# Kernel optimization log

Hardware: AMD Instinct MI355X
Metric: run time of the kernel (lower is better)

Reference implementation:

```python
import jax, jax.numpy as jnp
import numpy as np

N_NEURONS = 100000
NNZ = 3200000
N_SENSORY = 5000
BATCH = 16
NUM_LAYERS = 8
THRESHOLD = 0.01
TANH_STEEPNESS = 5.0


def setup_inputs() -> dict:
    key = jax.random.key(0)
    k1, k2, k3, k4 = jax.random.split(key, 4)
    inputs = jax.random.uniform(k1, (BATCH, N_SENSORY, NUM_LAYERS), dtype=jnp.float32)
    # sparse connectome in COO form; small values so activations stay in a sane range
    weight_vals = jax.random.normal(k2, (NNZ,), dtype=jnp.float32) * 0.1
    weight_rows = jax.random.randint(k3, (NNZ,), 0, N_NEURONS, dtype=jnp.int32)
    weight_cols = jax.random.randint(k4, (NNZ,), 0, N_NEURONS, dtype=jnp.int32)
    sensory_indices = jnp.arange(N_SENSORY, dtype=jnp.int32)
    return {
        "inputs": inputs,
        "weight_vals": weight_vals,
        "weight_rows": weight_rows,
        "weight_cols": weight_cols,
        "sensory_indices": sensory_indices,
    }


def _spmm(vals, rows, cols, x):
    # x: (N, B); y[r, b] = sum_{e: rows[e]==r} vals[e] * x[cols[e], b]
    return jax.ops.segment_sum(vals[:, None] * x[cols], rows, num_segments=N_NEURONS)


def _activate(y):
    y = jnp.where(y >= THRESHOLD, y, jnp.zeros_like(y))
    return jnp.tanh(TANH_STEEPNESS * y)


def reference(inputs, weight_vals, weight_rows, weight_cols, sensory_indices):
    B, S, T = inputs.shape  # T == num_layers
    # preprocess sensory input: threshold then clamp to <= 1
    inp = jnp.where(inputs >= THRESHOLD, inputs, jnp.zeros_like(inputs))
    inp = jnp.minimum(inp, jnp.ones_like(inp))
    # state x: (N, B)
    full_input = jnp.zeros((N_NEURONS, B), inputs.dtype).at[sensory_indices].add(inp[:, :, 0].T)
    x = _activate(_spmm(weight_vals, weight_rows, weight_cols, full_input))
    acts = []
    for layer in range(1, T):
        # inject sensory input for this time step and clamp to <= 1
        x = x.at[sensory_indices].add(inp[:, :, layer].T)
        x = jnp.minimum(x, jnp.ones_like(x))
        acts.append(x)
        x = _activate(_spmm(weight_vals, weight_rows, weight_cols, x))
    acts.append(x)  # last layer: no injection
    # (T, N, B) -> (B, N, T), matching torch vmap'd cat along time dim
    return jnp.stack(acts, axis=0).transpose(2, 1, 0)
```

## Files before the change

### kernel.cpp

```cpp
#include <hip/hip_runtime.h>


#define N_NEURONS 100000
#define NNZ_CNT   3200000
#define N_SENSORY 5000
#define BATCH     16
#define T_LAYERS  8
#define THRESH    0.01f
#define STEEP     5.0f

#define NB (N_NEURONS * BATCH)
#define NT (N_NEURONS * T_LAYERS)
#define ST (N_SENSORY * T_LAYERS)

#define FXS32     134217728.0f
#define FXI32     7.450580596923828e-9f

#define LBITS   9
#define BROWS   (1 << LBITS)
#define NBUCKET ((N_NEURONS + BROWS - 1) / BROWS)
#define EPB     4096
#define NBLK_A  ((NNZ_CNT + EPB - 1) / EPB)

#define FXSCALE   17592186044416.0f
#define FXINV     (1.0 / 17592186044416.0)

__device__ __forceinline__ float thresh_clamp_inp(float u) {
    u = (u >= THRESH) ? u : 0.0f;
    return fminf(u, 1.0f);
}
__device__ __forceinline__ float activate(float y) {
    y = (y >= THRESH) ? y : 0.0f;
    return tanhf(STEEP * y);
}


__global__ void k_init(const float* __restrict__ inp, float* __restrict__ state0,
                       int* __restrict__ btotal) {
    int i = blockIdx.x * blockDim.x + threadIdx.x;
    if (i >= NB) return;
    int n = i >> 4, b = i & 15;
    float v = 0.0f;
    if (n < N_SENSORY) v = thresh_clamp_inp(inp[b * ST + n * T_LAYERS + 0]);
    state0[i] = v;
    if (i < NBUCKET) btotal[i] = 0;
}

__global__ void __launch_bounds__(1024) k_bcount(const int* __restrict__ rows,
                                                 int* __restrict__ btotal) {
    __shared__ int cnt[NBUCKET];
    const int e0 = blockIdx.x * EPB;
    for (int i = threadIdx.x; i < NBUCKET; i += 1024) cnt[i] = 0;
    __syncthreads();
    #pragma unroll
    for (int i = 0; i < EPB / 1024; ++i) {
        int e = e0 + i * 1024 + threadIdx.x;
        if (e < NNZ_CNT) atomicAdd(&cnt[rows[e] >> LBITS], 1);
    }
    __syncthreads();
    for (int i = threadIdx.x; i < NBUCKET; i += 1024)
        if (cnt[i]) atomicAdd(&btotal[i], cnt[i]);
}

__global__ void k_bscan(const int* __restrict__ btotal, int* __restrict__ bbase,
                        int* __restrict__ bcur, int* __restrict__ row_ptr) {
    __shared__ int lds[256];
    int tid = threadIdx.x;
    int v = (tid < NBUCKET) ? btotal[tid] : 0;
    lds[tid] = v;
    __syncthreads();
    for (int off = 1; off < 256; off <<= 1) {
        int add = (tid >= off) ? lds[tid - off] : 0;
        __syncthreads();
        lds[tid] += add;
        __syncthreads();
    }
    if (tid < NBUCKET) {
        bbase[tid] = lds[tid] - v;
        bcur[tid]  = lds[tid] - v;
    }
    if (tid == 0) { bbase[NBUCKET] = NNZ_CNT; row_ptr[N_NEURONS] = NNZ_CNT; }
}

__global__ void __launch_bounds__(1024) k_passA(const float* __restrict__ vals,
                                                const int* __restrict__ rows,
                                                const int* __restrict__ cols,
                                                int* bcur,
                                                int2* __restrict__ slab) {
    __shared__ int cnt[NBUCKET];
    __shared__ int base[NBUCKET];
    const int e0 = blockIdx.x * EPB;
    for (int i = threadIdx.x; i < NBUCKET; i += 1024) cnt[i] = 0;
    __syncthreads();
    #pragma unroll
    for (int i = 0; i < EPB / 1024; ++i) {
        int e = e0 + i * 1024 + threadIdx.x;
        if (e < NNZ_CNT) atomicAdd(&cnt[rows[e] >> LBITS], 1);
    }
    __syncthreads();
    for (int i = threadIdx.x; i < NBUCKET; i += 1024) {
        int c = cnt[i];
        base[i] = (c > 0) ? atomicAdd(&bcur[i], c) : 0;
        cnt[i] = 0;
    }
    __syncthreads();
    #pragma unroll
    for (int i = 0; i < EPB / 1024; ++i) {
        int e = e0 + i * 1024 + threadIdx.x;
        if (e < NNZ_CNT) {
            int r = rows[e];
            int k = r >> LBITS;
            int pos = base[k] + atomicAdd(&cnt[k], 1);
            slab[pos] = make_int2((cols[e] << LBITS) | (r & (BROWS - 1)),
                                  __float_as_int(vals[e] * FXS32));
        }
    }
}

__global__ void __launch_bounds__(1024) k_passB(const int* __restrict__ bbase,
                                                const int2* __restrict__ slab,
                                                int2* __restrict__ packed,
                                                int* __restrict__ row_ptr) {
    __shared__ int cnt[BROWS];
    __shared__ int scn[BROWS];
    const int tid = threadIdx.x;
    const int k  = blockIdx.x;
    const int r0 = k * BROWS;
    const int nr = min(BROWS, N_NEURONS - r0);
    const int P0 = bbase[k], P1 = bbase[k + 1];
    for (int i = tid; i < BROWS; i += 1024) cnt[i] = 0;
    __syncthreads();
    for (int i = P0 + tid; i < P1; i += 1024)
        atomicAdd(&cnt[slab[i].x & (BROWS - 1)], 1);
    __syncthreads();
    if (tid < BROWS) scn[tid] = cnt[tid];
    __syncthreads();
    for (int off = 1; off < BROWS; off <<= 1) {
        int add = (tid < BROWS && tid >= off) ? scn[tid - off] : 0;
        __syncthreads();
        if (tid < BROWS) scn[tid] += add;
        __syncthreads();
    }
    if (tid < BROWS) {
        int ex = P0 + scn[tid] - cnt[tid];
        if (tid < nr) row_ptr[r0 + tid] = ex;
        scn[tid] = ex;
    }
    __syncthreads();
    for (int i = P0 + tid; i < P1; i += 1024) {
        int2 pe = slab[i];
        int d = atomicAdd(&scn[pe.x & (BROWS - 1)], 1);
        packed[d] = make_int2(pe.x >> LBITS, pe.y);
    }
}

__global__ void __launch_bounds__(256) k_layer(const int* __restrict__ row_ptr,
                                               const int2* __restrict__ packed,
                                               const float* __restrict__ state_in,
                                               const float* __restrict__ inp,
                                               float* __restrict__ plane_out,
                                               int t) {
    __shared__ int2 ebuf[16][17];
    const int tid = threadIdx.x;
    const int g = tid >> 4, b = tid & 15;
    const int r = blockIdx.x * 16 + g;
    const int s = row_ptr[r], e = row_ptr[r + 1];
    int acc = 0;
    for (int base = s; base < e; base += 16) {
        int idx = base + b;
        int2 pe = (idx < e) ? packed[idx] : make_int2(0, 0);
        ebuf[g][b] = pe;
        #pragma unroll
        for (int j = 0; j < 16; ++j) {
            int2 q = ebuf[g][j];
            float prod = __int_as_float(q.y) * state_in[q.x * BATCH + b];
            acc += __float2int_rn(prod);
        }
    }
    float y = (float)acc * FXI32;
    float a = activate(y);
    if (t < T_LAYERS - 1) {
        if (r < N_SENSORY) a += thresh_clamp_inp(inp[b * ST + r * T_LAYERS + (t + 1)]);
        a = fminf(a, 1.0f);
    }
    plane_out[r * BATCH + b] = a;
}

__global__ void k_out(const float* __restrict__ planes, float* __restrict__ out) {
    int i = blockIdx.x * blockDim.x + threadIdx.x;
    if (i >= NB) return;
    int n = i >> 4, b = i & 15;
    float4 o0, o1;
    o0.x = planes[0 * NB + i]; o0.y = planes[1 * NB + i];
    o0.z = planes[2 * NB + i]; o0.w = planes[3 * NB + i];
    o1.x = planes[4 * NB + i]; o1.y = planes[5 * NB + i];
    o1.z = planes[6 * NB + i]; o1.w = planes[7 * NB + i];
    float4* dst = (float4*)&out[b * NT + n * T_LAYERS];
    dst[0] = o0; dst[1] = o1;
}

__global__ void k2_init(const float* __restrict__ inp, float* __restrict__ state,
                        long long* __restrict__ acc) {
    int stride = gridDim.x * blockDim.x;
    for (int i = blockIdx.x * blockDim.x + threadIdx.x; i < NB; i += stride) {
        int n = i >> 4, b = i & 15;
        float v = 0.0f;
        if (n < N_SENSORY) v = thresh_clamp_inp(inp[b * ST + n * T_LAYERS + 0]);
        state[i] = v;
        acc[i]   = 0LL;
    }
}
__global__ void __launch_bounds__(256) k2_spmm(const float* __restrict__ vals,
                                               const int* __restrict__ rows,
                                               const int* __restrict__ cols,
                                               const float* __restrict__ state,
                                               long long* acc) {
    int tid = blockIdx.x * blockDim.x + threadIdx.x;
    int b = tid & 15;
    int e = tid >> 4;
    int estride = (gridDim.x * blockDim.x) >> 4;
    for (; e < NNZ_CNT; e += estride) {
        float xv = state[cols[e] * BATCH + b];
        long long fx = llrintf(vals[e] * xv * FXSCALE);
        if (fx != 0LL)
            atomicAdd((unsigned long long*)&acc[rows[e] * BATCH + b], (unsigned long long)fx);
    }
}
__global__ void k2_act_inject(long long* acc, const float* __restrict__ inp,
                              float* __restrict__ state, float* __restrict__ out, int t) {
    int stride = gridDim.x * blockDim.x;
    for (int i = blockIdx.x * blockDim.x + threadIdx.x; i < NB; i += stride) {
        int n = i >> 4, b = i & 15;
        float y = (float)((double)acc[i] * FXINV);
        acc[i] = 0LL;
        float v = activate(y);
        if (n < N_SENSORY) v += thresh_clamp_inp(inp[b * ST + n * T_LAYERS + (t + 1)]);
        v = fminf(v, 1.0f);
        state[i] = v;
        out[b * NT + n * T_LAYERS + t] = v;
    }
}
__global__ void k2_act_final(const long long* __restrict__ acc, float* __restrict__ out) {
    int stride = gridDim.x * blockDim.x;
    for (int i = blockIdx.x * blockDim.x + threadIdx.x; i < NB; i += stride) {
        int n = i >> 4, b = i & 15;
        float y = (float)((double)acc[i] * FXINV);
        out[b * NT + n * T_LAYERS + (T_LAYERS - 1)] = activate(y);
    }
}

extern "C" void kernel_launch(void* const* d_in, const int* in_sizes, int n_in,
                              void* d_out, int out_size, void* d_ws, size_t ws_size,
                              hipStream_t stream) {
    const float* inputs = (const float*)d_in[0];
    const float* vals   = (const float*)d_in[1];
    const int*   rows   = (const int*)  d_in[2];
    const int*   cols   = (const int*)  d_in[3];
    float* out = (float*)d_out;

    const size_t sz_planes = (size_t)T_LAYERS * NB * 4;
    const size_t sz_packed = (size_t)NNZ_CNT * 8;
    const size_t sz_rowptr = ((size_t)N_NEURONS + 2) * 4;
    const size_t sz_bt     = (size_t)(NBUCKET + 8) * 4;
    const size_t REQ = sz_planes + sz_packed + sz_rowptr + 3 * sz_bt;

    const int block = 256;

    if (ws_size >= REQ) {
        char* ws = (char*)d_ws;
        float* planes  = (float*)ws;
        int2*  packed  = (int2*)(ws + sz_planes);
        int*   row_ptr = (int*)(ws + sz_planes + sz_packed);
        int*   btotal  = (int*)(ws + sz_planes + sz_packed + sz_rowptr);
        int*   bbase   = (int*)(ws + sz_planes + sz_packed + sz_rowptr + sz_bt);
        int*   bcur    = (int*)(ws + sz_planes + sz_packed + sz_rowptr + 2 * sz_bt);
        float* state0  = planes + (size_t)(T_LAYERS - 1) * NB;
        int2*  slab    = (int2*)planes;

        const int grid_nb = (NB + block - 1) / block;

        k_init<<<grid_nb, block, 0, stream>>>(inputs, state0, btotal);
        k_bcount<<<NBLK_A, 1024, 0, stream>>>(rows, btotal);
        k_bscan<<<1, 256, 0, stream>>>(btotal, bbase, bcur, row_ptr);
        k_passA<<<NBLK_A, 1024, 0, stream>>>(vals, rows, cols, bcur, slab);
        k_passB<<<NBUCKET, 1024, 0, stream>>>(bbase, slab, packed, row_ptr);

        for (int t = 0; t < T_LAYERS; ++t) {
            const float* sin_ = (t == 0) ? state0 : planes + (size_t)(t - 1) * NB;
            k_layer<<<grid_nb, block, 0, stream>>>(row_ptr, packed, sin_, inputs,
                                                   planes + (size_t)t * NB, t);
        }
        k_out<<<grid_nb, block, 0, stream>>>(planes, out);
    } else {
        long long* acc   = (long long*)d_ws;
        float*     state = (float*)(acc + NB);
        const int grid_ew = 2048, grid_sp = 2048;
        k2_init<<<grid_ew, block, 0, stream>>>(inputs, state, acc);
        for (int t = 0; t < T_LAYERS; ++t) {
            k2_spmm<<<grid_sp, block, 0, stream>>>(vals, rows, cols, state, acc);
            if (t < T_LAYERS - 1)
                k2_act_inject<<<grid_ew, block, 0, stream>>>(acc, inputs, state, out, t);
            else
                k2_act_final<<<grid_ew, block, 0, stream>>>(acc, out);
        }
    }
}
```

Baseline: 400.8 us.

## Assign one wavefront per row in SpMM layer kernel with shuffle reduction

The layer kernel now maps a full 64-lane wavefront to each row. Four edge groups of 16 batch lanes each load edges directly from global memory, and their integer partial sums are combined with xor shuffles, replacing the shared-memory staging of 16 edges per 16-lane group. This is meant to give more memory-level parallelism per row (about 32 nonzeros per row) and remove the LDS round trips and padded iterations. In exchange it launches four times as many wavefronts per row, and only a quarter of the lanes do the final store.

```diff
diff --git a/kernel.cpp b/kernel.cpp
--- a/kernel.cpp
+++ b/kernel.cpp
@@ -160,30 +160,38 @@
                                                const float* __restrict__ inp,
                                                float* __restrict__ plane_out,
                                                int t) {
-    __shared__ int2 ebuf[16][17];
     const int tid = threadIdx.x;
-    const int g = tid >> 4, b = tid & 15;
-    const int r = blockIdx.x * 16 + g;
+    const int ln  = tid & 63;
+    const int jj  = ln >> 4;
+    const int b   = ln & 15;
+    const int r   = blockIdx.x * 4 + (tid >> 6);
     const int s = row_ptr[r], e = row_ptr[r + 1];
     int acc = 0;
-    for (int base = s; base < e; base += 16) {
-        int idx = base + b;
-        int2 pe = (idx < e) ? packed[idx] : make_int2(0, 0);
-        ebuf[g][b] = pe;
+    int base = s;
+    for (; base + 16 <= e; base += 16) {
         #pragma unroll
-        for (int j = 0; j < 16; ++j) {
-            int2 q = ebuf[g][j];
-            float prod = __int_as_float(q.y) * state_in[q.x * BATCH + b];
-            acc += __float2int_rn(prod);
-        }
-    }
-    float y = (float)acc * FXI32;
-    float a = activate(y);
-    if (t < T_LAYERS - 1) {
-        if (r < N_SENSORY) a += thresh_clamp_inp(inp[b * ST + r * T_LAYERS + (t + 1)]);
-        a = fminf(a, 1.0f);
-    }
-    plane_out[r * BATCH + b] = a;
+        for (int k = 0; k < 4; ++k) {
+            int2 q = packed[base + k * 4 + jj];
+            acc += __float2int_rn(__int_as_float(q.y) * state_in[(q.x << 4) + b]);
+        }
+    }
+    for (; base < e; base += 4) {
+        int idx = base + jj;
+        if (idx < e) {
+            int2 q = packed[idx];
+            acc += __float2int_rn(__int_as_float(q.y) * state_in[(q.x << 4) + b]);
+        }
+    }
+    acc += __shfl_xor(acc, 16, 64);
+    acc += __shfl_xor(acc, 32, 64);
+    if (jj == 0) {
+        float a = activate((float)acc * FXI32);
+        if (t < T_LAYERS - 1) {
+            if (r < N_SENSORY) a += thresh_clamp_inp(inp[b * ST + r * T_LAYERS + (t + 1)]);
+            a = fminf(a, 1.0f);
+        }
+        plane_out[(r << 4) + b] = a;
+    }
 }
 
 __global__ void k_out(const float* __restrict__ planes, float* __restrict__ out) {
@@ -278,6 +286,7 @@
         int2*  slab    = (int2*)planes;
 
         const int grid_nb = (NB + block - 1) / block;
+        const int grid_ly = N_NEURONS / 4;
 
         k_init<<<grid_nb, block, 0, stream>>>(inputs, state0, btotal);
         k_bcount<<<NBLK_A, 1024, 0, stream>>>(rows, btotal);
@@ -287,7 +296,7 @@
 
         for (int t = 0; t < T_LAYERS; ++t) {
             const float* sin_ = (t == 0) ? state0 : planes + (size_t)(t - 1) * NB;
-            k_layer<<<grid_nb, block, 0, stream>>>(row_ptr, packed, sin_, inputs,
+            k_layer<<<grid_ly, block, 0, stream>>>(row_ptr, packed, sin_, inputs,
                                                    planes + (size_t)t * NB, t);
         }
         k_out<<<grid_nb, block, 0, stream>>>(planes, out);
```

Result: slower. 578.7 us (+44.4%).
